# Performance work log

Hardware: AMD Instinct MI355X
Metric: run time of the kernel (lower is better)

Reference implementation:

```python
import jax, jax.numpy as jnp
import numpy as np

N = 8192
IN_F = 128
OUT_F = 128
ALPHA = 0.2  # LeakyReLU negative slope
NEG_INF = -9e15


def setup_inputs() -> dict:
    key = jax.random.key(0)
    k1, k2, k3, k4 = jax.random.split(key, 4)
    h = jax.random.normal(k1, (N, IN_F), dtype=jnp.float32)
    adj = jax.random.randint(k2, (N, N), 0, 2, dtype=jnp.int32)
    # nn.Linear(in, out, bias=False).weight is (out, in); store as (in, out) for h @ W
    W = jax.random.normal(k3, (IN_F, OUT_F), dtype=jnp.float32) * (1.0 / np.sqrt(IN_F))
    # a: (2*out_features, 1), xavier_uniform with gain=1.414
    limit = 1.414 * np.sqrt(6.0 / (2 * OUT_F + 1))
    a = jax.random.uniform(k4, (2 * OUT_F, 1), dtype=jnp.float32, minval=-limit, maxval=limit)
    return {"h": h, "adj": adj, "W": W, "a": a}


def reference(h, adj, W, a):
    Wh = h @ W  # (N, OUT_F)
    a1 = a[:OUT_F, 0]   # score contribution from source node i
    a2 = a[OUT_F:, 0]   # score contribution from target node j
    # e_ij = leakyrelu(Wh_i . a1 + Wh_j . a2) -- avoids the O(N^2 * 2F) concat
    s1 = Wh @ a1  # (N,)
    s2 = Wh @ a2  # (N,)
    e = jax.nn.leaky_relu(s1[:, None] + s2[None, :], negative_slope=ALPHA)  # (N, N)
    masked = jnp.where(adj > 0, e, NEG_INF)
    attention = jax.nn.softmax(masked, axis=1)  # (N, N)
    # dropout is a no-op in eval mode
    h_prime = attention @ Wh  # (N, OUT_F)
    return jax.nn.elu(h_prime)  # concat=True -> ELU
```

## Files before the change

kernel.cpp:

```cpp
#include <hip/hip_runtime.h>
#include <cstdint>
#include <cstddef>


#define NROW 8192
#define FDIM 128

typedef _Float16 f16;
typedef f16 f16x8 __attribute__((ext_vector_type(8)));
typedef float f32x4 __attribute__((ext_vector_type(4)));
typedef float f32x16 __attribute__((ext_vector_type(16)));

#define WS_BP  (2u*1024u*1024u)
#define WS_S12 (4u*1024u*1024u)
#define WS_RC  (WS_S12 + 64u*1024u)
#define WS_EF  (WS_RC + 128u*1024u)
#define WS_M2  (WS_EF + 64u*1024u)
#define WS_PWS (WS_M2 + 4u*1024u)

__global__ __launch_bounds__(256) void kA_wh(const float* __restrict__ h,
                                             const float* __restrict__ W,
                                             const float* __restrict__ a,
                                             f16* __restrict__ Bp,
                                             float2* __restrict__ s12,
                                             float* __restrict__ M2v) {
  __shared__ float smem[4736];
  const int bid = (int)blockIdx.x;
  const int t = (int)threadIdx.x;

  const int rb = bid * 32;
  const f32x4* hv = (const f32x4*)(h + (size_t)rb * FDIM);
#pragma unroll
  for (int i = 0; i < 4; ++i) {
    int fidx = t + i * 256;
    f32x4 v = hv[fidx];
    int e0 = fidx * 4;
    int r = e0 >> 7, k = e0 & 127;
    smem[(k + 0) * 36 + r] = v[0];
    smem[(k + 1) * 36 + r] = v[1];
    smem[(k + 2) * 36 + r] = v[2];
    smem[(k + 3) * 36 + r] = v[3];
  }
  __syncthreads();
  const int f = t & 127, rh = t >> 7;
  f32x4 z = {0.f, 0.f, 0.f, 0.f};
  f32x4 acc0 = z, acc1 = z, acc2 = z, acc3 = z;
  for (int k = 0; k < 128; ++k) {
    float w = W[k * FDIM + f];
    const f32x4* hp = (const f32x4*)(smem + k * 36 + rh * 16);
    acc0 += hp[0] * w;
    acc1 += hp[1] * w;
    acc2 += hp[2] * w;
    acc3 += hp[3] * w;
  }
  union { f16 hx[16]; uint4 u[2]; } pk;
#pragma unroll
  for (int q = 0; q < 4; ++q) {
    pk.hx[0 + q]  = (f16)acc0[q];
    pk.hx[4 + q]  = (f16)acc1[q];
    pk.hx[8 + q]  = (f16)acc2[q];
    pk.hx[12 + q] = (f16)acc3[q];
  }
  f16* bdst = Bp + ((size_t)((bid * 2 + rh) * 4 + (f >> 5)) * 64 + (f & 31)) * 8;
  *(uint4*)bdst = pk.u[0];
  *(uint4*)(bdst + 256) = pk.u[1];

  __syncthreads();
#pragma unroll
  for (int q = 0; q < 4; ++q) {
    smem[(rh * 16 + 0  + q) * 132 + f] = acc0[q];
    smem[(rh * 16 + 4  + q) * 132 + f] = acc1[q];
    smem[(rh * 16 + 8  + q) * 132 + f] = acc2[q];
    smem[(rh * 16 + 12 + q) * 132 + f] = acc3[q];
  }
  __syncthreads();
  {
    const int row = t & 31, fc = t >> 5;
    const float* wrow = smem + row * 132 + fc * 16;
    float s1 = 0.f, s2 = 0.f;
#pragma unroll
    for (int ff = 0; ff < 16; ++ff) {
      float wv = wrow[ff];
      int fg = fc * 16 + ff;
      s1 = fmaf(wv, a[fg], s1);
      s2 = fmaf(wv, a[128 + fg], s2);
    }
    float* part = smem + 4224;
    part[0 * 256 + fc * 32 + row] = s1;
    part[1 * 256 + fc * 32 + row] = s2;
    __syncthreads();
    if (t < 32) {
      float s1t = 0.f, s2t = 0.f;
#pragma unroll
      for (int c2 = 0; c2 < 8; ++c2) {
        s1t += part[c2 * 32 + t];
        s2t += part[256 + c2 * 32 + t];
      }
      s12[rb + t] = make_float2(s1t, s2t);
      float mx = s2t;
#pragma unroll
      for (int off = 16; off; off >>= 1) mx = fmaxf(mx, __shfl_xor(mx, off, 64));
      if (t == 0) M2v[bid] = mx;
    }
  }
}

__global__ __launch_bounds__(256) void k1c_prep(const float2* __restrict__ s12,
                                                const float* __restrict__ M2v,
                                                float4* __restrict__ RC,
                                                float2* __restrict__ EF) {
  __shared__ float red[4];
  const int t = (int)threadIdx.x;
  float v = M2v[t];
#pragma unroll
  for (int off = 32; off; off >>= 1) v = fmaxf(v, __shfl_xor(v, off, 64));
  if ((t & 63) == 0) red[t >> 6] = v;
  __syncthreads();
  float M2 = fmaxf(fmaxf(red[0], red[1]), fmaxf(red[2], red[3]));
  int j = (int)blockIdx.x * 256 + t;
  float2 s = s12[j];
  float c = s.x + M2;
  c = fmaxf(c, 0.2f * c);
  RC[j] = make_float4(__expf(-s.x), __expf(s.x - c), __expf(0.2f * s.x - c), 0.f);
  EF[j] = make_float2(__expf(s.y), __expf(0.2f * s.y));
}

__global__ __launch_bounds__(256) void k2_main(const int* __restrict__ adj,
                                               const f16* __restrict__ Bp,
                                               const float4* __restrict__ RC,
                                               const float* __restrict__ EF,
                                               float* __restrict__ Pws,
                                               float* __restrict__ Dws,
                                               int jspan) {
  const int tid = (int)threadIdx.x;
  const int L = tid & 63, w = tid >> 6;
  const int wid = (int)blockIdx.x * 4 + w;
  const int rg = wid & 255;
  const int c = wid >> 8;
  const int rb = rg * 32;
  const int m = L & 31, kb = L >> 5;
  const int row = rb + m;
  const int j0 = c * jspan;
  const int niter = jspan >> 5;

  const float4 rc = RC[row];
  const float tau = rc.x, kap1 = rc.y, kap2 = rc.z;

  const int* arow = adj + (size_t)(rb + (L >> 3)) * NROW + j0 + 4 * (L & 7);
  const f32x4* ep = (const f32x4*)(EF + 2 * (j0 + kb * 8));
  const f16* bp = Bp + (size_t)(j0 >> 4) * 2048 + L * 8;

  int4 A0n = *(const int4*)(arow);
  int4 A1n = *(const int4*)(arow + 8 * NROW);
  int4 A2n = *(const int4*)(arow + 16 * NROW);
  int4 A3n = *(const int4*)(arow + 24 * NROW);
  f32x4 E0 = ep[0], E1 = ep[1], E2 = ep[2], E3 = ep[3];
  f32x4 E4 = ep[8], E5 = ep[9], E6 = ep[10], E7 = ep[11];

  f32x16 zz = {0.f};
  f32x16 acc[4] = {zz, zz, zz, zz};
  float dloc = 0.f;

  const int shmt = 4 * (L & 7);
  const int srcl = 8 * (L & 7) + ((L >> 3) & 7);

  for (int it = 0; it < niter; ++it) {
    const f16* bt = bp + (size_t)it * 4096;
    f16x8 B00 = *(const f16x8*)(bt);
    f16x8 B01 = *(const f16x8*)(bt + 512);
    f16x8 B02 = *(const f16x8*)(bt + 1024);
    f16x8 B03 = *(const f16x8*)(bt + 1536);
    f16x8 B10 = *(const f16x8*)(bt + 2048);
    f16x8 B11 = *(const f16x8*)(bt + 2560);
    f16x8 B12 = *(const f16x8*)(bt + 3072);
    f16x8 B13 = *(const f16x8*)(bt + 3584);

    int4 A0 = A0n, A1 = A1n, A2 = A2n, A3 = A3n;
    int nxo = ((it + 1 < niter) ? (it + 1) : it) * 32;
    A0n = *(const int4*)(arow + nxo);
    A1n = *(const int4*)(arow + 8 * NROW + nxo);
    A2n = *(const int4*)(arow + 16 * NROW + nxo);
    A3n = *(const int4*)(arow + 24 * NROW + nxo);

    unsigned W0 = ((A0.x > 0 ? 1u : 0u) | (A0.y > 0 ? 2u : 0u) |
                   (A0.z > 0 ? 4u : 0u) | (A0.w > 0 ? 8u : 0u)) << shmt;
    unsigned W1 = ((A1.x > 0 ? 1u : 0u) | (A1.y > 0 ? 2u : 0u) |
                   (A1.z > 0 ? 4u : 0u) | (A1.w > 0 ? 8u : 0u)) << shmt;
    unsigned W2 = ((A2.x > 0 ? 1u : 0u) | (A2.y > 0 ? 2u : 0u) |
                   (A2.z > 0 ? 4u : 0u) | (A2.w > 0 ? 8u : 0u)) << shmt;
    unsigned W3 = ((A3.x > 0 ? 1u : 0u) | (A3.y > 0 ? 2u : 0u) |
                   (A3.z > 0 ? 4u : 0u) | (A3.w > 0 ? 8u : 0u)) << shmt;
    W0 |= (unsigned)__shfl_xor((int)W0, 1, 64);
    W1 |= (unsigned)__shfl_xor((int)W1, 1, 64);
    W2 |= (unsigned)__shfl_xor((int)W2, 1, 64);
    W3 |= (unsigned)__shfl_xor((int)W3, 1, 64);
    W0 |= (unsigned)__shfl_xor((int)W0, 2, 64);
    W1 |= (unsigned)__shfl_xor((int)W1, 2, 64);
    W2 |= (unsigned)__shfl_xor((int)W2, 2, 64);
    W3 |= (unsigned)__shfl_xor((int)W3, 2, 64);
    W0 |= (unsigned)__shfl_xor((int)W0, 4, 64);
    W1 |= (unsigned)__shfl_xor((int)W1, 4, 64);
    W2 |= (unsigned)__shfl_xor((int)W2, 4, 64);
    W3 |= (unsigned)__shfl_xor((int)W3, 4, 64);
    unsigned a01 = (L & 1) ? W1 : W0;
    unsigned a23 = (L & 1) ? W3 : W2;
    unsigned wsel = (L & 2) ? a23 : a01;
    unsigned WD = (unsigned)__shfl((int)wsel, srcl, 64);

    const unsigned u0 = WD >> (kb * 8);
    const unsigned u1 = u0 >> 16;
    f16x8 af0, af1;
    {
      float p;
      p = (E0[0] > tau) ? E0[0] * kap1 : E0[1] * kap2; p = (u0 & 1u)   ? p : 0.f; dloc += p; af0[0] = (f16)p;
      p = (E0[2] > tau) ? E0[2] * kap1 : E0[3] * kap2; p = (u0 & 2u)   ? p : 0.f; dloc += p; af0[1] = (f16)p;
      p = (E1[0] > tau) ? E1[0] * kap1 : E1[1] * kap2; p = (u0 & 4u)   ? p : 0.f; dloc += p; af0[2] = (f16)p;
      p = (E1[2] > tau) ? E1[2] * kap1 : E1[3] * kap2; p = (u0 & 8u)   ? p : 0.f; dloc += p; af0[3] = (f16)p;
      p = (E2[0] > tau) ? E2[0] * kap1 : E2[1] * kap2; p = (u0 & 16u)  ? p : 0.f; dloc += p; af0[4] = (f16)p;
      p = (E2[2] > tau) ? E2[2] * kap1 : E2[3] * kap2; p = (u0 & 32u)  ? p : 0.f; dloc += p; af0[5] = (f16)p;
      p = (E3[0] > tau) ? E3[0] * kap1 : E3[1] * kap2; p = (u0 & 64u)  ? p : 0.f; dloc += p; af0[6] = (f16)p;
      p = (E3[2] > tau) ? E3[2] * kap1 : E3[3] * kap2; p = (u0 & 128u) ? p : 0.f; dloc += p; af0[7] = (f16)p;
      p = (E4[0] > tau) ? E4[0] * kap1 : E4[1] * kap2; p = (u1 & 1u)   ? p : 0.f; dloc += p; af1[0] = (f16)p;
      p = (E4[2] > tau) ? E4[2] * kap1 : E4[3] * kap2; p = (u1 & 2u)   ? p : 0.f; dloc += p; af1[1] = (f16)p;
      p = (E5[0] > tau) ? E5[0] * kap1 : E5[1] * kap2; p = (u1 & 4u)   ? p : 0.f; dloc += p; af1[2] = (f16)p;
      p = (E5[2] > tau) ? E5[2] * kap1 : E5[3] * kap2; p = (u1 & 8u)   ? p : 0.f; dloc += p; af1[3] = (f16)p;
      p = (E6[0] > tau) ? E6[0] * kap1 : E6[1] * kap2; p = (u1 & 16u)  ? p : 0.f; dloc += p; af1[4] = (f16)p;
      p = (E6[2] > tau) ? E6[2] * kap1 : E6[3] * kap2; p = (u1 & 32u)  ? p : 0.f; dloc += p; af1[5] = (f16)p;
      p = (E7[0] > tau) ? E7[0] * kap1 : E7[1] * kap2; p = (u1 & 64u)  ? p : 0.f; dloc += p; af1[6] = (f16)p;
      p = (E7[2] > tau) ? E7[2] * kap1 : E7[3] * kap2; p = (u1 & 128u) ? p : 0.f; dloc += p; af1[7] = (f16)p;
    }

    int adv = (it < niter - 1) ? 1 : 0;
    ep += adv * 16;
    E0 = ep[0]; E1 = ep[1]; E2 = ep[2]; E3 = ep[3];
    E4 = ep[8]; E5 = ep[9]; E6 = ep[10]; E7 = ep[11];

    __builtin_amdgcn_s_setprio(1);
    acc[0] = __builtin_amdgcn_mfma_f32_32x32x16_f16(af0, B00, acc[0], 0, 0, 0);
    acc[1] = __builtin_amdgcn_mfma_f32_32x32x16_f16(af0, B01, acc[1], 0, 0, 0);
    acc[2] = __builtin_amdgcn_mfma_f32_32x32x16_f16(af0, B02, acc[2], 0, 0, 0);
    acc[3] = __builtin_amdgcn_mfma_f32_32x32x16_f16(af0, B03, acc[3], 0, 0, 0);
    acc[0] = __builtin_amdgcn_mfma_f32_32x32x16_f16(af1, B10, acc[0], 0, 0, 0);
    acc[1] = __builtin_amdgcn_mfma_f32_32x32x16_f16(af1, B11, acc[1], 0, 0, 0);
    acc[2] = __builtin_amdgcn_mfma_f32_32x32x16_f16(af1, B12, acc[2], 0, 0, 0);
    acc[3] = __builtin_amdgcn_mfma_f32_32x32x16_f16(af1, B13, acc[3], 0, 0, 0);
    __builtin_amdgcn_s_setprio(0);
  }

  dloc += __shfl_xor(dloc, 32, 64);
  if (L < 32) Dws[(size_t)c * NROW + row] = dloc;

  float* P = Pws + ((size_t)c * NROW + rb) * FDIM + (L & 31);
#pragma unroll
  for (int nt = 0; nt < 4; ++nt) {
#pragma unroll
    for (int reg = 0; reg < 16; ++reg) {
      int rr = (reg & 3) + 8 * (reg >> 2) + 4 * kb;
      P[(size_t)rr * FDIM + nt * 32] = acc[nt][reg];
    }
  }
}

__global__ __launch_bounds__(256) void k3_comb(const float* __restrict__ Pws,
                                               const float* __restrict__ Dws,
                                               float* __restrict__ out, int S) {
  int g = (int)blockIdx.x * 256 + (int)threadIdx.x;
  int r = g >> 5, f4 = g & 31;
  f32x4 s = {0.f, 0.f, 0.f, 0.f};
  float den = 0.f;
  for (int c2 = 0; c2 < S; ++c2) {
    s += *(const f32x4*)(Pws + ((size_t)c2 * NROW + r) * FDIM + f4 * 4);
    den += Dws[(size_t)c2 * NROW + r];
  }
  float inv = 1.0f / den;
  f32x4 o;
#pragma unroll
  for (int e = 0; e < 4; ++e) {
    float x = s[e] * inv;
    o[e] = x > 0.f ? x : expm1f(x);
  }
  *(f32x4*)(out + (size_t)r * FDIM + f4 * 4) = o;
}

extern "C" void kernel_launch(void* const* d_in, const int* in_sizes, int n_in,
                              void* d_out, int out_size, void* d_ws, size_t ws_size,
                              hipStream_t stream) {
  const float* h = (const float*)d_in[0];
  const int* adj = (const int*)d_in[1];
  const float* W = (const float*)d_in[2];
  const float* a = (const float*)d_in[3];
  float* out = (float*)d_out;
  char* ws = (char*)d_ws;
  f16* Bp = (f16*)(ws + WS_BP);
  float2* s12 = (float2*)(ws + WS_S12);
  float4* RC = (float4*)(ws + WS_RC);
  float2* EF = (float2*)(ws + WS_EF);
  float* M2v = (float*)(ws + WS_M2);

  const size_t partial_bytes = (size_t)NROW * FDIM * 4;
  int S = (ws_size >= WS_PWS + 8 * partial_bytes + 8 * (size_t)NROW * 4) ? 8 : 2;
  float* Pws = (float*)(ws + WS_PWS);
  float* Dws = (float*)(ws + WS_PWS + (size_t)S * partial_bytes);
  int jspan = NROW / S;

  kA_wh<<<dim3(256), dim3(256), 0, stream>>>(h, W, a, Bp, s12, M2v);
  k1c_prep<<<dim3(32), dim3(256), 0, stream>>>(s12, M2v, RC, EF);
  k2_main<<<dim3(64 * S), dim3(256), 0, stream>>>(adj, Bp, RC, (const float*)EF, Pws, Dws, jspan);
  k3_comb<<<dim3(1024), dim3(256), 0, stream>>>(Pws, Dws, out, S);
}
```

Measured before the change: 451.4 us.

## Deepen adjacency prefetch to two iterations and cap k2_main occupancy

The adjacency-tile loads in the main attention kernel now run two iterations ahead, using ping-pong register sets in a loop unrolled by two. The next loads are issued right after the mask bits are extracted, so the consuming registers are reused at once. This aims to hide more global-memory latency on the dominant adj stream. The launch bounds also request at least 2 blocks per CU, which limits registers and could cause spills given the extra live int4 sets. The unrolled loop assumes niter is even.

Result: no change. 452.1 us (+0.2%).

```diff
diff --git a/kernel.cpp b/kernel.cpp
--- a/kernel.cpp
+++ b/kernel.cpp
@@ -125,13 +125,13 @@
   EF[j] = make_float2(__expf(s.y), __expf(0.2f * s.y));
 }
 
-__global__ __launch_bounds__(256) void k2_main(const int* __restrict__ adj,
-                                               const f16* __restrict__ Bp,
-                                               const float4* __restrict__ RC,
-                                               const float* __restrict__ EF,
-                                               float* __restrict__ Pws,
-                                               float* __restrict__ Dws,
-                                               int jspan) {
+__global__ __launch_bounds__(256, 2) void k2_main(const int* __restrict__ adj,
+                                                  const f16* __restrict__ Bp,
+                                                  const float4* __restrict__ RC,
+                                                  const float* __restrict__ EF,
+                                                  float* __restrict__ Pws,
+                                                  float* __restrict__ Dws,
+                                                  int jspan) {
   const int tid = (int)threadIdx.x;
   const int L = tid & 63, w = tid >> 6;
   const int wid = (int)blockIdx.x * 4 + w;
@@ -150,10 +150,6 @@
   const f32x4* ep = (const f32x4*)(EF + 2 * (j0 + kb * 8));
   const f16* bp = Bp + (size_t)(j0 >> 4) * 2048 + L * 8;
 
-  int4 A0n = *(const int4*)(arow);
-  int4 A1n = *(const int4*)(arow + 8 * NROW);
-  int4 A2n = *(const int4*)(arow + 16 * NROW);
-  int4 A3n = *(const int4*)(arow + 24 * NROW);
   f32x4 E0 = ep[0], E1 = ep[1], E2 = ep[2], E3 = ep[3];
   f32x4 E4 = ep[8], E5 = ep[9], E6 = ep[10], E7 = ep[11];
 
@@ -164,8 +160,18 @@
   const int shmt = 4 * (L & 7);
   const int srcl = 8 * (L & 7) + ((L >> 3) & 7);
 
-  for (int it = 0; it < niter; ++it) {
-    const f16* bt = bp + (size_t)it * 4096;
+  int4 Pa0 = *(const int4*)(arow);
+  int4 Pa1 = *(const int4*)(arow + 8 * NROW);
+  int4 Pa2 = *(const int4*)(arow + 16 * NROW);
+  int4 Pa3 = *(const int4*)(arow + 24 * NROW);
+  const int o1 = 32;
+  int4 Pb0 = *(const int4*)(arow + o1);
+  int4 Pb1 = *(const int4*)(arow + 8 * NROW + o1);
+  int4 Pb2 = *(const int4*)(arow + 16 * NROW + o1);
+  int4 Pb3 = *(const int4*)(arow + 24 * NROW + o1);
+
+  auto body = [&](int4& A0, int4& A1, int4& A2, int4& A3, int ro,
+                  const f16* bt, int adv) {
     f16x8 B00 = *(const f16x8*)(bt);
     f16x8 B01 = *(const f16x8*)(bt + 512);
     f16x8 B02 = *(const f16x8*)(bt + 1024);
@@ -175,13 +181,6 @@
     f16x8 B12 = *(const f16x8*)(bt + 3072);
     f16x8 B13 = *(const f16x8*)(bt + 3584);
 
-    int4 A0 = A0n, A1 = A1n, A2 = A2n, A3 = A3n;
-    int nxo = ((it + 1 < niter) ? (it + 1) : it) * 32;
-    A0n = *(const int4*)(arow + nxo);
-    A1n = *(const int4*)(arow + 8 * NROW + nxo);
-    A2n = *(const int4*)(arow + 16 * NROW + nxo);
-    A3n = *(const int4*)(arow + 24 * NROW + nxo);
-
     unsigned W0 = ((A0.x > 0 ? 1u : 0u) | (A0.y > 0 ? 2u : 0u) |
                    (A0.z > 0 ? 4u : 0u) | (A0.w > 0 ? 8u : 0u)) << shmt;
     unsigned W1 = ((A1.x > 0 ? 1u : 0u) | (A1.y > 0 ? 2u : 0u) |
@@ -190,6 +189,11 @@
                    (A2.z > 0 ? 4u : 0u) | (A2.w > 0 ? 8u : 0u)) << shmt;
     unsigned W3 = ((A3.x > 0 ? 1u : 0u) | (A3.y > 0 ? 2u : 0u) |
                    (A3.z > 0 ? 4u : 0u) | (A3.w > 0 ? 8u : 0u)) << shmt;
+    A0 = *(const int4*)(arow + ro);
+    A1 = *(const int4*)(arow + 8 * NROW + ro);
+    A2 = *(const int4*)(arow + 16 * NROW + ro);
+    A3 = *(const int4*)(arow + 24 * NROW + ro);
+
     W0 |= (unsigned)__shfl_xor((int)W0, 1, 64);
     W1 |= (unsigned)__shfl_xor((int)W1, 1, 64);
     W2 |= (unsigned)__shfl_xor((int)W2, 1, 64);
@@ -230,7 +234,6 @@
       p = (E7[2] > tau) ? E7[2] * kap1 : E7[3] * kap2; p = (u1 & 128u) ? p : 0.f; dloc += p; af1[7] = (f16)p;
     }
 
-    int adv = (it < niter - 1) ? 1 : 0;
     ep += adv * 16;
     E0 = ep[0]; E1 = ep[1]; E2 = ep[2]; E3 = ep[3];
     E4 = ep[8]; E5 = ep[9]; E6 = ep[10]; E7 = ep[11];
@@ -245,6 +248,15 @@
     acc[2] = __builtin_amdgcn_mfma_f32_32x32x16_f16(af1, B12, acc[2], 0, 0, 0);
     acc[3] = __builtin_amdgcn_mfma_f32_32x32x16_f16(af1, B13, acc[3], 0, 0, 0);
     __builtin_amdgcn_s_setprio(0);
+  };
+
+  for (int it = 0; it < niter; it += 2) {
+    int r2 = it + 2; if (r2 > niter - 1) r2 = niter - 1;
+    int r3 = it + 3; if (r3 > niter - 1) r3 = niter - 1;
+    body(Pa0, Pa1, Pa2, Pa3, r2 * 32, bp + (size_t)it * 4096,
+         (it < niter - 1) ? 1 : 0);
+    body(Pb0, Pb1, Pb2, Pb3, r3 * 32, bp + (size_t)(it + 1) * 4096,
+         (it + 1 < niter - 1) ? 1 : 0);
   }
 
   dloc += __shfl_xor(dloc, 32, 64);
```
